# Kernel optimization log

Hardware: AMD Instinct MI355X
Metric: run time of the kernel (lower is better)

## Reference

```python
import jax, jax.numpy as jnp
import numpy as np
from jax import lax

V, E, H, L, WE = 21128, 300, 256, 15, 5
B, T = 64, 256


def _lstm(x, Wih, Whh, bih, bhh):
    # x: [B, T, D]; PyTorch gate order i, f, g, o
    b, t, _ = x.shape
    h0 = jnp.zeros((b, Whh.shape[1]), x.dtype)
    c0 = jnp.zeros_like(h0)
    xs = jnp.swapaxes(x, 0, 1)  # [T, B, D]

    def step(carry, xt):
        h, c = carry
        g = xt @ Wih.T + h @ Whh.T + (bih + bhh)
        i, f, gg, o = jnp.split(g, 4, axis=-1)
        c = jax.nn.sigmoid(f) * c + jax.nn.sigmoid(i) * jnp.tanh(gg)
        h = jax.nn.sigmoid(o) * jnp.tanh(c)
        return (h, c), h

    _, hs = lax.scan(step, (h0, c0), xs)
    return jnp.swapaxes(hs, 0, 1)  # [B, T, H]


def _bilstm_emissions(input_ids, lengths, softword_ids, emb, soft_emb,
                      Wih_f, Whh_f, bih_f, bhh_f, Wih_b, Whh_b, bih_b, bhh_b,
                      Wlin, blin):
    x = jnp.concatenate([emb[input_ids], soft_emb[softword_ids]], axis=-1)  # [B,T,2E]
    h_f = _lstm(x, Wih_f, Whh_f, bih_f, bhh_f)
    # backward direction: per-sequence reverse over valid length (packed-seq semantics)
    t_idx = jnp.arange(x.shape[1])[None, :]
    rev = jnp.where(t_idx < lengths[:, None], lengths[:, None] - 1 - t_idx, t_idx)
    x_rev = jnp.take_along_axis(x, rev[:, :, None], axis=1)
    h_r = _lstm(x_rev, Wih_b, Whh_b, bih_b, bhh_b)
    h_b = jnp.take_along_axis(h_r, rev[:, :, None], axis=1)
    h = jnp.concatenate([h_f, h_b], axis=-1)  # [B,T,2H]
    return h @ Wlin.T + blin  # [B,T,L]


def _crf_nll(emissions, tags, mask, start_t, end_t, trans):
    # mask: [B,T] float, mask[:,0] == 1
    fmask = mask
    # numerator: score of the gold path
    em = jnp.take_along_axis(emissions, tags[:, :, None], axis=2)[:, :, 0]  # [B,T]
    em_score = jnp.sum(em * fmask, axis=1)
    tr_score = jnp.sum(trans[tags[:, :-1], tags[:, 1:]] * fmask[:, 1:], axis=1)
    lengths = jnp.sum(fmask, axis=1).astype(jnp.int32)
    last_tags = jnp.take_along_axis(tags, (lengths - 1)[:, None], axis=1)[:, 0]
    num = start_t[tags[:, 0]] + em_score + tr_score + end_t[last_tags]
    # denominator: forward algorithm (log-partition)
    alpha0 = start_t[None, :] + emissions[:, 0]  # [B,L]

    def step(alpha, inp):
        e_t, m_t = inp  # [B,L], [B]
        nxt = jax.nn.logsumexp(alpha[:, :, None] + trans[None] + e_t[:, None, :], axis=1)
        alpha = jnp.where(m_t[:, None] > 0, nxt, alpha)
        return alpha, None

    es = jnp.swapaxes(emissions[:, 1:], 0, 1)  # [T-1,B,L]
    ms = jnp.swapaxes(fmask[:, 1:], 0, 1)      # [T-1,B]
    alpha, _ = lax.scan(step, alpha0, (es, ms))
    den = jax.nn.logsumexp(alpha + end_t[None, :], axis=1)
    llh = jnp.sum(num - den)  # torchcrf reduction='sum'
    return -llh


def setup_inputs() -> dict:
    key = jax.random.key(0)
    ks = jax.random.split(key, 20)
    s = 1.0 / np.sqrt(H)
    inp = {
        "input_ids": jax.random.randint(ks[0], (B, T), 0, V),
        "lengths": jax.random.randint(ks[1], (B,), 64, T + 1),
        "softword_ids": jax.random.randint(ks[2], (B, T), 0, WE),
        "label_ids": jax.random.randint(ks[3], (B, T), 0, L),
        "emb": jax.random.normal(ks[4], (V, E), jnp.float32) * 0.1,
        "soft_emb": jax.random.normal(ks[5], (WE, E), jnp.float32),
        "Wih_f": jax.random.uniform(ks[6], (4 * H, 2 * E), jnp.float32, -s, s),
        "Whh_f": jax.random.uniform(ks[7], (4 * H, H), jnp.float32, -s, s),
        "bih_f": jax.random.uniform(ks[8], (4 * H,), jnp.float32, -s, s),
        "bhh_f": jax.random.uniform(ks[9], (4 * H,), jnp.float32, -s, s),
        "Wih_b": jax.random.uniform(ks[10], (4 * H, 2 * E), jnp.float32, -s, s),
        "Whh_b": jax.random.uniform(ks[11], (4 * H, H), jnp.float32, -s, s),
        "bih_b": jax.random.uniform(ks[12], (4 * H,), jnp.float32, -s, s),
        "bhh_b": jax.random.uniform(ks[13], (4 * H,), jnp.float32, -s, s),
        "Wlin": jax.random.uniform(ks[14], (L, 2 * H), jnp.float32, -s, s),
        "blin": jax.random.uniform(ks[15], (L,), jnp.float32, -s, s),
        "start_t": jax.random.uniform(ks[16], (L,), jnp.float32, -0.1, 0.1),
        "end_t": jax.random.uniform(ks[17], (L,), jnp.float32, -0.1, 0.1),
        "trans": jax.random.uniform(ks[18], (L, L), jnp.float32, -0.1, 0.1),
    }
    return inp


def reference(input_ids, lengths, softword_ids, label_ids, emb, soft_emb,
              Wih_f, Whh_f, bih_f, bhh_f, Wih_b, Whh_b, bih_b, bhh_b,
              Wlin, blin, start_t, end_t, trans):
    emissions = _bilstm_emissions(input_ids, lengths, softword_ids, emb, soft_emb,
                                  Wih_f, Whh_f, bih_f, bhh_f,
                                  Wih_b, Whh_b, bih_b, bhh_b, Wlin, blin)
    mask = (jnp.arange(emissions.shape[1])[None, :] < lengths[:, None]).astype(emissions.dtype)
    return _crf_nll(emissions, label_ids, mask, start_t, end_t, trans)
```

## Files before the change

kernel.cpp:

```cpp
#include <hip/hip_runtime.h>
#include <hip/hip_bf16.h>

#define BB 64
#define TT 256
#define HH 256
#define LL 15
#define E300 300
#define KPAD 608
#define NG 2048
#define MROWS 16384

typedef float  floatx4 __attribute__((ext_vector_type(4)));
typedef float  floatx2 __attribute__((ext_vector_type(2)));
typedef __bf16 bf16x8  __attribute__((ext_vector_type(8)));



__global__ void k_embed(const int* __restrict__ ids, const int* __restrict__ sids,
                        const float* __restrict__ emb,
                        const float* __restrict__ semb,
                        __hip_bfloat16* __restrict__ X) {
    int row = blockIdx.x;
    int id  = ids[row];
    int sid = sids[row];
    const float* e0 = emb  + (long)id  * E300;
    const float* e1 = semb + (long)sid * E300;
    __hip_bfloat16* xr = X + (long)row * KPAD;
    for (int c = threadIdx.x; c < KPAD; c += blockDim.x) {
        float v;
        if (c < 300)      v = e0[c];
        else if (c < 600) v = e1[c - 300];
        else              v = 0.f;
        xr[c] = __float2bfloat16(v);
    }
}

__global__ void k_wcat(const float* __restrict__ Wf,
                       const float* __restrict__ Wb,
                       __hip_bfloat16* __restrict__ Wcat) {
    int r = blockIdx.x;
    int dir = r >> 10, rr = r & 1023, j = rr >> 2, gate = rr & 3;
    const float* src = (dir ? Wb : Wf) + (long)(gate * 256 + j) * 600;
    __hip_bfloat16* dst = Wcat + (long)r * KPAD;
    for (int c = threadIdx.x; c < KPAD; c += blockDim.x)
        dst[c] = __float2bfloat16((c < 600) ? src[c] : 0.f);
}

__global__ void k_wpk(const float* __restrict__ Wf,
                      const float* __restrict__ Wb,
                      unsigned int* __restrict__ Wpk8) {
    int d = blockIdx.x >> 8;
    int k = blockIdx.x & 255;
    int j = threadIdx.x;
    const float* W = d ? Wb : Wf;
    float w0 = W[((long)(0 * 256 + j)) * 256 + k] * 16.f;
    float w1 = W[((long)(1 * 256 + j)) * 256 + k] * 16.f;
    float w2 = W[((long)(2 * 256 + j)) * 256 + k] * 16.f;
    float w3 = W[((long)(3 * 256 + j)) * 256 + k] * 16.f;
    int r = 0;
    r = __builtin_amdgcn_cvt_pk_fp8_f32(w0, w1, r, false);
    r = __builtin_amdgcn_cvt_pk_fp8_f32(w2, w3, r, true);
    Wpk8[(((long)d * 4 + (k >> 6)) * 256 + j) * 64 + (k & 63)] = (unsigned int)r;
}

__global__ void k_bias(const float* __restrict__ bfi, const float* __restrict__ bfh,
                       const float* __restrict__ bbi, const float* __restrict__ bbh,
                       float* __restrict__ bias) {
    int i = blockIdx.x * blockDim.x + threadIdx.x;
    if (i < 2048) {
        int d = i >> 10, j = i & 1023;
        const float* b1 = d ? bbi : bfi;
        const float* b2 = d ? bbh : bfh;
        bias[i] = b1[j] + b2[j];
    }
}

__global__ __launch_bounds__(256) void k_gemm(const __hip_bfloat16* __restrict__ A,
                                              const __hip_bfloat16* __restrict__ Bw,
                                              __hip_bfloat16* __restrict__ C) {
    __shared__ __align__(16) unsigned short As[128 * 40];
    __shared__ __align__(16) unsigned short Bs[128 * 40];
    int bm = blockIdx.x, bn = blockIdx.y;
    int row0 = bm * 128, col0 = bn * 128;
    int tid = threadIdx.x;
    int wave = tid >> 6, lane = tid & 63;
    int wm = (wave >> 1) * 64, wn = (wave & 1) * 64;
    int l15 = lane & 15, quad = lane >> 4;
    floatx4 acc[4][4];
    #pragma unroll
    for (int i = 0; i < 4; ++i)
        #pragma unroll
        for (int j = 0; j < 4; ++j) acc[i][j] = (floatx4){0.f, 0.f, 0.f, 0.f};

    int r1 = tid >> 2, p1 = tid & 3;

    for (int kk = 0; kk < KPAD; kk += 32) {
        uint4 a0 = *(const uint4*)(A  + ((long)(row0 + r1))      * KPAD + kk + p1 * 8);
        uint4 a1 = *(const uint4*)(A  + ((long)(row0 + 64 + r1)) * KPAD + kk + p1 * 8);
        uint4 b0 = *(const uint4*)(Bw + ((long)(col0 + r1))      * KPAD + kk + p1 * 8);
        uint4 b1 = *(const uint4*)(Bw + ((long)(col0 + 64 + r1)) * KPAD + kk + p1 * 8);
        *(uint4*)&As[r1 * 40 + p1 * 8]        = a0;
        *(uint4*)&As[(64 + r1) * 40 + p1 * 8] = a1;
        *(uint4*)&Bs[r1 * 40 + p1 * 8]        = b0;
        *(uint4*)&Bs[(64 + r1) * 40 + p1 * 8] = b1;
        __syncthreads();
        bf16x8 af[4], bfr[4];
        #pragma unroll
        for (int tm = 0; tm < 4; ++tm)
            af[tm] = *(const bf16x8*)&As[(wm + tm * 16 + l15) * 40 + quad * 8];
        #pragma unroll
        for (int tn = 0; tn < 4; ++tn)
            bfr[tn] = *(const bf16x8*)&Bs[(wn + tn * 16 + l15) * 40 + quad * 8];
        #pragma unroll
        for (int tm = 0; tm < 4; ++tm)
            #pragma unroll
            for (int tn = 0; tn < 4; ++tn)
                acc[tm][tn] = __builtin_amdgcn_mfma_f32_16x16x32_bf16(af[tm], bfr[tn], acc[tm][tn], 0, 0, 0);
        __syncthreads();
    }
    #pragma unroll
    for (int tm = 0; tm < 4; ++tm)
        #pragma unroll
        for (int tn = 0; tn < 4; ++tn) {
            int m0 = row0 + wm + tm * 16 + quad * 4;
            int n  = col0 + wn + tn * 16 + l15;
            #pragma unroll
            for (int r = 0; r < 4; ++r)
                C[((long)(m0 + r)) * NG + n] = __float2bfloat16(acc[tm][tn][r]);
        }
}

#define MAC1(w, hk) {                                                   \
    floatx2 wif = __builtin_amdgcn_cvt_pk_f32_fp8((w), false);          \
    floatx2 wgo = __builtin_amdgcn_cvt_pk_f32_fp8((w), true);           \
    floatx2 h2 = (floatx2){(hk), (hk)};                                 \
    aIF += h2 * wif;                                                    \
    aGO += h2 * wgo; }

#define MACW(W, base) {                                                 \
    floatx4 h4 = *(const floatx4*)&hq[(base)];                          \
    MAC1((W).x, h4[0]); MAC1((W).y, h4[1]);                             \
    MAC1((W).z, h4[2]); MAC1((W).w, h4[3]); }

#define MACL(g) {                                                       \
    floatx4 h4 = *(const floatx4*)&hq[16 + 4 * (g)];                    \
    unsigned long long wa = *(volatile const unsigned long long*)&Wl[(2 * (g)) * 256];     \
    unsigned long long wb = *(volatile const unsigned long long*)&Wl[(2 * (g) + 1) * 256]; \
    MAC1((unsigned)wa, h4[0]); MAC1((unsigned)(wa >> 32), h4[1]);       \
    MAC1((unsigned)wb, h4[2]); MAC1((unsigned)(wb >> 32), h4[3]); }

__device__ __forceinline__ float b2f(unsigned u) {
    union { unsigned i; float f; } v; v.i = u << 16; return v.f;
}

__global__ __launch_bounds__(1024)
void k_lstm(const __hip_bfloat16* __restrict__ G,
            const unsigned int* __restrict__ Wpk8,
            const float* __restrict__ bias,
            const int* __restrict__ lengths,
            __hip_bfloat16* __restrict__ Hout) {
    int dir = blockIdx.x & 1;
    int b   = blockIdx.x >> 1;
    int tid = threadIdx.x;
    int q   = tid >> 8;
    int j   = tid & 255;
    __shared__ __align__(16) float hs[HH];
    __shared__ __align__(16) float red[4][HH][4];
    __shared__ __align__(16) float bls[4][HH];
    __shared__ __align__(16) unsigned long long Wlds[64 * 256];
    float c = 0.f;
    if (tid < HH) {
        const float* bs = bias + dir * 1024;
        bls[0][j] = bs[j];
        bls[1][j] = bs[256 + j];
        bls[2][j] = bs[512 + j];
        bls[3][j] = bs[768 + j];
        hs[j] = 0.f;
    }
    int len = lengths[b];
    const float* hq = hs + q * 64;
    const uint4* wt = (const uint4*)Wpk8 + (((long)dir * 4 + q) * 256 + j) * 16;
    uint4 W00 = wt[0], W01 = wt[1], W02 = wt[2], W03 = wt[3];
    unsigned long long* Wl = Wlds + q * 16 * 256 + j;
    #pragma unroll
    for (int i = 0; i < 8; ++i) {
        uint4 v = wt[4 + i];
        Wl[(2 * i) * 256]     = (unsigned long long)v.x | ((unsigned long long)v.y << 32);
        Wl[(2 * i + 1) * 256] = (unsigned long long)v.z | ((unsigned long long)v.w << 32);
    }
    unsigned long wsa = (unsigned long)(wt + 12);
    const __hip_bfloat16* Gb = G + ((long)b * TT) * NG + dir * 1024;
    __syncthreads();
    for (int t = 0; t < TT; ++t) {
        int tt = t;
        if (dir) tt = (t < len) ? (len - 1 - t) : t;
        unsigned long wsv = wsa;
        asm volatile("" : "+v"(wsv));
        const uint4* ws = (const uint4*)wsv;
        uint4 S0 = ws[0], S1 = ws[1], S2 = ws[2], S3 = ws[3];
        uint2 gp = (uint2){0u, 0u};
        if (tid < HH)
            gp = *(const uint2*)(Gb + (long)tt * NG + j * 4);
        floatx2 aIF = (floatx2){0.f, 0.f};
        floatx2 aGO = (floatx2){0.f, 0.f};
        MACW(W00, 0) MACW(W01, 4) MACW(W02, 8) MACW(W03, 12)
        MACL(0) MACL(1) MACL(2) MACL(3)
        MACL(4) MACL(5) MACL(6) MACL(7)
        MACW(S0, 48) MACW(S1, 52) MACW(S2, 56) MACW(S3, 60)
        *(floatx4*)&red[q][j][0] = (floatx4){aIF[0], aIF[1], aGO[0], aGO[1]};
        __syncthreads();
        if (tid < HH) {
            floatx4 r0 = *(const floatx4*)&red[0][j][0];
            floatx4 r1 = *(const floatx4*)&red[1][j][0];
            floatx4 r2 = *(const floatx4*)&red[2][j][0];
            floatx4 r3 = *(const floatx4*)&red[3][j][0];
            float ai = bls[0][j] + b2f(gp.x & 0xffffu)  + r0[0] + r1[0] + r2[0] + r3[0];
            float af = bls[1][j] + b2f(gp.x >> 16)      + r0[1] + r1[1] + r2[1] + r3[1];
            float ag = bls[2][j] + b2f(gp.y & 0xffffu)  + r0[2] + r1[2] + r2[2] + r3[2];
            float ao = bls[3][j] + b2f(gp.y >> 16)      + r0[3] + r1[3] + r2[3] + r3[3];
            float ii = 1.f / (1.f + __expf(-ai));
            float ff = 1.f / (1.f + __expf(-af));
            float gg = tanhf(ag);
            float oo = 1.f / (1.f + __expf(-ao));
            c = ff * c + ii * gg;
            float h = oo * tanhf(c);
            hs[j] = h * 0.0625f;
            Hout[((long)(b * TT + tt)) * 512 + dir * HH + j] = __float2bfloat16(h);
        }
        __syncthreads();
    }
}

__global__ void k_emis(const __hip_bfloat16* __restrict__ Hc,
                       const float* __restrict__ Wlin,
                       const float* __restrict__ blin,
                       float* __restrict__ E) {
    int gid = blockIdx.x * blockDim.x + threadIdx.x;
    if (gid >= MROWS * LL) return;
    int row = gid / LL;
    int l = gid - row * LL;
    const __hip_bfloat16* hr = Hc + (long)row * 512;
    const float* wr = Wlin + l * 512;
    float s = blin[l];
    #pragma unroll 8
    for (int k = 0; k < 512; ++k)
        s = fmaf(__bfloat162float(hr[k]), wr[k], s);
    E[gid] = s;
}

__global__ void k_crf(const float* __restrict__ E,
                      const int* __restrict__ tags,
                      const int* __restrict__ lengths,
                      const float* __restrict__ start_t,
                      const float* __restrict__ end_t,
                      const float* __restrict__ trans,
                      float* __restrict__ outp) {
    int b = blockIdx.x;
    int lane = threadIdx.x;
    int len = lengths[b];
    const float* Eb = E + (long)b * TT * LL;
    const int* tg = tags + b * TT;
    float tcol[LL];
    #pragma unroll
    for (int k = 0; k < LL; ++k)
        tcol[k] = (lane < LL) ? trans[k * LL + lane] : 0.f;
    float alpha = (lane < LL) ? start_t[lane] + Eb[lane] : -1e30f;
    for (int t = 1; t < len; ++t) {
        float e = (lane < LL) ? Eb[t * LL + lane] : 0.f;
        float m = -1e30f;
        float v[LL];
        #pragma unroll
        for (int k = 0; k < LL; ++k) {
            float ak = __shfl(alpha, k, 64);
            v[k] = ak + tcol[k];
            m = fmaxf(m, v[k]);
        }
        float s = 0.f;
        #pragma unroll
        for (int k = 0; k < LL; ++k) s += __expf(v[k] - m);
        alpha = m + __logf(s) + e;
    }
    float z = alpha + ((lane < LL) ? end_t[lane] : -1e30f);
    float m2 = -1e30f;
    #pragma unroll
    for (int k = 0; k < LL; ++k) m2 = fmaxf(m2, __shfl(z, k, 64));
    float s2 = 0.f;
    #pragma unroll
    for (int k = 0; k < LL; ++k) s2 += __expf(__shfl(z, k, 64) - m2);
    float den = m2 + __logf(s2);
    float part = 0.f;
    for (int t = lane; t < TT; t += 64) {
        if (t < len) {
            int tag = tg[t];
            part += Eb[t * LL + tag];
            if (t >= 1) part += trans[tg[t - 1] * LL + tag];
        }
    }
    #pragma unroll
    for (int off = 32; off > 0; off >>= 1) part += __shfl_down(part, off, 64);
    if (lane == 0) {
        float num = part + start_t[tg[0]] + end_t[tg[len - 1]];
        outp[b] = num - den;
    }
}

__global__ void k_final(const float* __restrict__ outp, float* __restrict__ out) {
    int lane = threadIdx.x;
    float v = outp[lane];
    #pragma unroll
    for (int off = 32; off > 0; off >>= 1) v += __shfl_down(v, off, 64);
    if (lane == 0) out[0] = -v;
}

extern "C" void kernel_launch(void* const* d_in, const int* in_sizes, int n_in,
                              void* d_out, int out_size, void* d_ws, size_t ws_size,
                              hipStream_t stream) {
    const int* input_ids    = (const int*)d_in[0];
    const int* lengths      = (const int*)d_in[1];
    const int* softword_ids = (const int*)d_in[2];
    const int* label_ids    = (const int*)d_in[3];
    const float* emb      = (const float*)d_in[4];
    const float* soft_emb = (const float*)d_in[5];
    const float* Wih_f = (const float*)d_in[6];
    const float* Whh_f = (const float*)d_in[7];
    const float* bih_f = (const float*)d_in[8];
    const float* bhh_f = (const float*)d_in[9];
    const float* Wih_b = (const float*)d_in[10];
    const float* Whh_b = (const float*)d_in[11];
    const float* bih_b = (const float*)d_in[12];
    const float* bhh_b = (const float*)d_in[13];
    const float* Wlin  = (const float*)d_in[14];
    const float* blin  = (const float*)d_in[15];
    const float* start_t = (const float*)d_in[16];
    const float* end_t   = (const float*)d_in[17];
    const float* trans   = (const float*)d_in[18];

    char* base = (char*)d_ws;
    float*          part = (float*)(base);
    float*          bias = (float*)(base + 256);
    float*          E    = (float*)(base + 8448);
    unsigned int*   Wpk8 = (unsigned int*)(base + 991488);
    __hip_bfloat16* Wcat = (__hip_bfloat16*)(base + 2040064);
    __hip_bfloat16* Hc   = (__hip_bfloat16*)(base + 4530432);
    __hip_bfloat16* X    = (__hip_bfloat16*)(base + 21307648);
    __hip_bfloat16* G    = (__hip_bfloat16*)(base + 41230592);

    k_embed<<<MROWS, 64, 0, stream>>>(input_ids, softword_ids, emb, soft_emb, X);
    k_wcat<<<NG, 64, 0, stream>>>(Wih_f, Wih_b, Wcat);
    k_wpk<<<512, 256, 0, stream>>>(Whh_f, Whh_b, Wpk8);
    k_bias<<<8, 256, 0, stream>>>(bih_f, bhh_f, bih_b, bhh_b, bias);
    k_gemm<<<dim3(MROWS / 128, NG / 128), 256, 0, stream>>>(X, Wcat, G);
    k_lstm<<<BB * 2, 1024, 0, stream>>>(G, Wpk8, bias, lengths, Hc);
    k_emis<<<(MROWS * LL) / 256, 256, 0, stream>>>(Hc, Wlin, blin, E);
    k_crf<<<BB, 64, 0, stream>>>(E, label_ids, lengths, start_t, end_t, trans, part);
    k_final<<<1, 64, 0, stream>>>(part, (float*)d_out);
}
```

Measured before the change: 1.520 ms.

## Reduce LSTM gate partials with wave shuffles and double-buffer hidden state

Remaps threads so that the four K-quarter partial sums for each hidden unit sit in the same wavefront, then reduces them with xor shuffles instead of a shared-memory scratch array. Double-buffering the hidden-state vector removes one of the two block barriers per timestep. Gate math now uses hardware reciprocal-based sigmoid and tanh, which adds some approximation error. The shared-memory weight layout is reindexed per wave and the hidden vector is padded to reduce bank conflicts.

```diff
diff --git a/kernel.cpp b/kernel.cpp
--- a/kernel.cpp
+++ b/kernel.cpp
@@ -144,13 +144,19 @@
 
 #define MACL(g) {                                                       \
     floatx4 h4 = *(const floatx4*)&hq[16 + 4 * (g)];                    \
-    unsigned long long wa = *(volatile const unsigned long long*)&Wl[(2 * (g)) * 256];     \
-    unsigned long long wb = *(volatile const unsigned long long*)&Wl[(2 * (g) + 1) * 256]; \
+    unsigned long long wa = *(volatile const unsigned long long*)&Wl[(2 * (g)) * 64];     \
+    unsigned long long wb = *(volatile const unsigned long long*)&Wl[(2 * (g) + 1) * 64]; \
     MAC1((unsigned)wa, h4[0]); MAC1((unsigned)(wa >> 32), h4[1]);       \
     MAC1((unsigned)wb, h4[2]); MAC1((unsigned)(wb >> 32), h4[3]); }
 
 __device__ __forceinline__ float b2f(unsigned u) {
     union { unsigned i; float f; } v; v.i = u << 16; return v.f;
+}
+__device__ __forceinline__ float sigm_(float x) {
+    return __builtin_amdgcn_rcpf(1.f + __expf(-x));
+}
+__device__ __forceinline__ float tanh_(float x) {
+    return 2.f * __builtin_amdgcn_rcpf(1.f + __expf(-2.f * x)) - 1.f;
 }
 
 __global__ __launch_bounds__(1024)
@@ -162,34 +168,33 @@
     int dir = blockIdx.x & 1;
     int b   = blockIdx.x >> 1;
     int tid = threadIdx.x;
-    int q   = tid >> 8;
-    int j   = tid & 255;
-    __shared__ __align__(16) float hs[HH];
-    __shared__ __align__(16) float red[4][HH][4];
-    __shared__ __align__(16) float bls[4][HH];
-    __shared__ __align__(16) unsigned long long Wlds[64 * 256];
-    float c = 0.f;
-    if (tid < HH) {
-        const float* bs = bias + dir * 1024;
-        bls[0][j] = bs[j];
-        bls[1][j] = bs[256 + j];
-        bls[2][j] = bs[512 + j];
-        bls[3][j] = bs[768 + j];
-        hs[j] = 0.f;
-    }
+    int w    = tid >> 6;
+    int lane = tid & 63;
+    int q    = lane >> 4;
+    int jj   = lane & 15;
+    int j    = w * 16 + jj;
+    __shared__ __align__(16) float hsbuf[2][4 * 68];
+    __shared__ __align__(16) unsigned long long Wlds[16 * 16 * 64];
+    if (tid < 2 * 4 * 68) ((float*)hsbuf)[tid] = 0.f;
     int len = lengths[b];
-    const float* hq = hs + q * 64;
     const uint4* wt = (const uint4*)Wpk8 + (((long)dir * 4 + q) * 256 + j) * 16;
     uint4 W00 = wt[0], W01 = wt[1], W02 = wt[2], W03 = wt[3];
-    unsigned long long* Wl = Wlds + q * 16 * 256 + j;
+    unsigned long long* Wl = Wlds + (long)w * 16 * 64 + lane;
     #pragma unroll
     for (int i = 0; i < 8; ++i) {
         uint4 v = wt[4 + i];
-        Wl[(2 * i) * 256]     = (unsigned long long)v.x | ((unsigned long long)v.y << 32);
-        Wl[(2 * i + 1) * 256] = (unsigned long long)v.z | ((unsigned long long)v.w << 32);
+        Wl[(2 * i) * 64]     = (unsigned long long)v.x | ((unsigned long long)v.y << 32);
+        Wl[(2 * i + 1) * 64] = (unsigned long long)v.z | ((unsigned long long)v.w << 32);
     }
     unsigned long wsa = (unsigned long)(wt + 12);
+    float bi = 0.f, bf_ = 0.f, bg = 0.f, bo = 0.f;
+    if (q == 0) {
+        const float* bs = bias + dir * 1024;
+        bi = bs[j]; bf_ = bs[256 + j]; bg = bs[512 + j]; bo = bs[768 + j];
+    }
     const __hip_bfloat16* Gb = G + ((long)b * TT) * NG + dir * 1024;
+    float c = 0.f;
+    int p = 0;
     __syncthreads();
     for (int t = 0; t < TT; ++t) {
         int tt = t;
@@ -199,35 +204,37 @@
         const uint4* ws = (const uint4*)wsv;
         uint4 S0 = ws[0], S1 = ws[1], S2 = ws[2], S3 = ws[3];
         uint2 gp = (uint2){0u, 0u};
-        if (tid < HH)
+        if (q == 0)
             gp = *(const uint2*)(Gb + (long)tt * NG + j * 4);
+        const float* hq = hsbuf[p] + q * 68;
         floatx2 aIF = (floatx2){0.f, 0.f};
         floatx2 aGO = (floatx2){0.f, 0.f};
         MACW(W00, 0) MACW(W01, 4) MACW(W02, 8) MACW(W03, 12)
         MACL(0) MACL(1) MACL(2) MACL(3)
         MACL(4) MACL(5) MACL(6) MACL(7)
         MACW(S0, 48) MACW(S1, 52) MACW(S2, 56) MACW(S3, 60)
-        *(floatx4*)&red[q][j][0] = (floatx4){aIF[0], aIF[1], aGO[0], aGO[1]};
-        __syncthreads();
-        if (tid < HH) {
-            floatx4 r0 = *(const floatx4*)&red[0][j][0];
-            floatx4 r1 = *(const floatx4*)&red[1][j][0];
-            floatx4 r2 = *(const floatx4*)&red[2][j][0];
-            floatx4 r3 = *(const floatx4*)&red[3][j][0];
-            float ai = bls[0][j] + b2f(gp.x & 0xffffu)  + r0[0] + r1[0] + r2[0] + r3[0];
-            float af = bls[1][j] + b2f(gp.x >> 16)      + r0[1] + r1[1] + r2[1] + r3[1];
-            float ag = bls[2][j] + b2f(gp.y & 0xffffu)  + r0[2] + r1[2] + r2[2] + r3[2];
-            float ao = bls[3][j] + b2f(gp.y >> 16)      + r0[3] + r1[3] + r2[3] + r3[3];
-            float ii = 1.f / (1.f + __expf(-ai));
-            float ff = 1.f / (1.f + __expf(-af));
-            float gg = tanhf(ag);
-            float oo = 1.f / (1.f + __expf(-ao));
-            c = ff * c + ii * gg;
-            float h = oo * tanhf(c);
-            hs[j] = h * 0.0625f;
+        if (q == 0) {
+            aIF += (floatx2){bi + b2f(gp.x & 0xffffu), bf_ + b2f(gp.x >> 16)};
+            aGO += (floatx2){bg + b2f(gp.y & 0xffffu), bo + b2f(gp.y >> 16)};
+        }
+        float ai = aIF[0], af = aIF[1], ag = aGO[0], ao = aGO[1];
+        ai += __shfl_xor(ai, 16, 64); af += __shfl_xor(af, 16, 64);
+        ag += __shfl_xor(ag, 16, 64); ao += __shfl_xor(ao, 16, 64);
+        ai += __shfl_xor(ai, 32, 64); af += __shfl_xor(af, 32, 64);
+        ag += __shfl_xor(ag, 32, 64); ao += __shfl_xor(ao, 32, 64);
+        float ii = sigm_(ai);
+        float ff = sigm_(af);
+        float gg = tanh_(ag);
+        float oo = sigm_(ao);
+        c = ff * c + ii * gg;
+        float h = oo * tanh_(c);
+        if (q == 0) {
+            hsbuf[p ^ 1][(j >> 6) * 68 + (j & 63)] = h * 0.0625f;
             Hout[((long)(b * TT + tt)) * 512 + dir * HH + j] = __float2bfloat16(h);
         }
-        __syncthreads();
+        p ^= 1;
+        asm volatile("s_waitcnt lgkmcnt(0)" ::: "memory");
+        __builtin_amdgcn_s_barrier();
     }
 }
 
```

New measurement: 1.554 ms. 2.2% more time.
